# Kernel optimization log

Hardware: AMD Instinct MI355X
Metric: run time of the kernel (lower is better)

## Reference

```python
import jax, jax.numpy as jnp
import numpy as np

B, S, D, H, F = 4, 2048, 1024, 16, 4096
HD = D // H
EPS = 1e-5


def _xavier(key, shape, fan_in, fan_out):
    a = float(np.sqrt(6.0 / (fan_in + fan_out)))
    return jax.random.uniform(key, shape, jnp.float32, -a, a)


def setup_inputs() -> dict:
    key = jax.random.key(0)
    ks = jax.random.split(key, 8)
    x = jax.random.normal(ks[0], (B, S, D), jnp.float32)
    # torch xavier_uniform on (1,H,D,HD) uses fan_in=D, fan_out=HD
    Wq = _xavier(ks[1], (H, D, HD), D, HD)
    Wk = _xavier(ks[2], (H, D, HD), D, HD)
    Wv = _xavier(ks[3], (H, D, HD), D, HD)
    Wo = _xavier(ks[4], (D, D), D, D)
    w_in = _xavier(ks[5], (D, F), D, F)
    b_in = jnp.zeros((F,), jnp.float32)
    w_out = _xavier(ks[6], (F, D), F, D)
    b_out = jnp.zeros((D,), jnp.float32)
    g1 = jnp.ones((D,), jnp.float32)
    be1 = jnp.zeros((D,), jnp.float32)
    g2 = jnp.ones((D,), jnp.float32)
    be2 = jnp.zeros((D,), jnp.float32)
    return {"x": x, "Wq": Wq, "Wk": Wk, "Wv": Wv, "Wo": Wo,
            "g1": g1, "be1": be1, "w_in": w_in, "b_in": b_in,
            "w_out": w_out, "b_out": b_out, "g2": g2, "be2": be2}


def _layernorm(x, g, b):
    mu = jnp.mean(x, axis=-1, keepdims=True)
    var = jnp.mean(jnp.square(x - mu), axis=-1, keepdims=True)
    return (x - mu) * jax.lax.rsqrt(var + EPS) * g + b


def reference(x, Wq, Wk, Wv, Wo, g1, be1, w_in, b_in, w_out, b_out, g2, be2):
    b, s, d = x.shape
    h, _, hd = Wq.shape
    q = jnp.einsum('bsd,hde->bhse', x, Wq)
    k = jnp.einsum('bsd,hde->bhse', x, Wk)
    v = jnp.einsum('bsd,hde->bhse', x, Wv)
    scores = jnp.einsum('bhse,bhte->bhst', q, k) / jnp.sqrt(jnp.float32(hd))
    causal = jnp.triu(jnp.ones((s, s), bool), k=1)  # [S,S]
    scores = jnp.where(causal, -jnp.inf, scores)
    p = jax.nn.softmax(scores, axis=-1)
    attn = jnp.einsum('bhst,bhte->bhse', p, v)
    # torch .view on contiguous (B,H,S,hd) -> (B,S,H*hd): plain reshape (no transpose)
    attn = attn.reshape(b, s, h * hd)
    attn = attn @ Wo
    x = _layernorm(x + attn, g1, be1)
    ffn = jax.nn.relu(x @ w_in + b_in) @ w_out + b_out
    x = _layernorm(x + ffn, g2, be2)
    return x
```

## Files before the change

### kernel.cpp

```cpp
#include <hip/hip_runtime.h>
#include <hip/hip_bf16.h>

typedef __hip_bfloat16 bf16;

#define BB 4
#define SS 2048
#define DD 1024
#define HH 16
#define FF 4096
#define HD 64
#define LN_EPS 1e-5f
#define QSCALE 0.1803368801111204f

typedef __attribute__((ext_vector_type(8))) __bf16 bf16x8;
typedef __attribute__((ext_vector_type(8))) unsigned short u16x8;
typedef __attribute__((ext_vector_type(4))) float f32x4;

__device__ __forceinline__ float cvt(float v) { return v; }
__device__ __forceinline__ float cvt(bf16 v) { return __bfloat162float(v); }
__device__ __forceinline__ void stf(float* p, float v) { *p = v; }
__device__ __forceinline__ void stf(bf16* p, float v) { *p = __float2bfloat16(v); }

__device__ __forceinline__ unsigned short f2bf_rne(float x) {
    unsigned int u = __float_as_uint(x);
    unsigned int r = (u + 0x7fffu + ((u >> 16) & 1u)) >> 16;
    return (unsigned short)r;
}

__device__ __forceinline__ void async_cp16(const void* g, void* l) {
    __builtin_amdgcn_global_load_lds(
        (const __attribute__((address_space(1))) unsigned int*)g,
        (__attribute__((address_space(3))) unsigned int*)l, 16, 0, 0);
}

__device__ __forceinline__ u16x8 ld_f32_chunk(const float* p) {
    const float4* q = (const float4*)p;
    const float4 a = q[0], b = q[1];
    u16x8 r;
    r[0] = f2bf_rne(a.x); r[1] = f2bf_rne(a.y); r[2] = f2bf_rne(a.z); r[3] = f2bf_rne(a.w);
    r[4] = f2bf_rne(b.x); r[5] = f2bf_rne(b.y); r[6] = f2bf_rne(b.z); r[7] = f2bf_rne(b.w);
    return r;
}

template <typename TA, typename TC, int EPI, int BW>
__launch_bounds__(256)
__global__ void mfma_gemm(const TA* __restrict__ A, const bf16* __restrict__ Bt,
                          TC* __restrict__ C, const float* __restrict__ bias,
                          const bf16* __restrict__ resb,
                          bf16* __restrict__ C2, bf16* __restrict__ C3,
                          int M, int N, int K, float oscale) {
    constexpr bool AF = (sizeof(TA) == 4);
    __shared__ unsigned short As[128 * 64];
    __shared__ unsigned short Bs[128 * 64];

    const int tid = threadIdx.x;
    const int lane = tid & 63;
    const int w = tid >> 6;
    const int wm = w >> 1, wn = w & 1;

    const int gx = gridDim.x, gy = gridDim.y;
    const int id = blockIdx.y * gx + blockIdx.x;
    const int R = gy >> 3;
    const int k = id & 7;
    const int j = id >> 3;
    const int sbs = R * BW;
    const int sb = j / sbs;
    const int rem = j % sbs;
    const int by = k * R + rem / BW;
    const int bx = sb * BW + rem % BW;
    const int m0 = by * 128, n0 = bx * 128;

    int ff[4], fr[4], fc[4], fg[4];
#pragma unroll
    for (int i = 0; i < 4; ++i) {
        ff[i] = tid + i * 256;
        fr[i] = ff[i] >> 3;
        fc[i] = ff[i] & 7;
        fg[i] = fc[i] ^ (fr[i] & 7);
    }

    f32x4 acc[4][4];
#pragma unroll
    for (int i = 0; i < 4; ++i)
#pragma unroll
        for (int j2 = 0; j2 < 4; ++j2) acc[i][j2] = (f32x4){0.f, 0.f, 0.f, 0.f};

    u16x8 sa[4];
    if (AF) {
#pragma unroll
        for (int i = 0; i < 4; ++i)
            sa[i] = ld_f32_chunk((const float*)A + (size_t)(m0 + fr[i]) * K + fg[i] * 8);
    }

    for (int k0 = 0; k0 < K; k0 += 64) {
        if (k0 > 0) __syncthreads();
        if (AF) {
#pragma unroll
            for (int i = 0; i < 4; ++i)
                *(u16x8*)&As[ff[i] * 8] = sa[i];
        } else {
#pragma unroll
            for (int i = 0; i < 4; ++i)
                async_cp16((const unsigned short*)A + (size_t)(m0 + fr[i]) * K + k0 + fg[i] * 8,
                           &As[ff[i] * 8]);
        }
#pragma unroll
        for (int i = 0; i < 4; ++i)
            async_cp16((const unsigned short*)Bt + (size_t)(n0 + fr[i]) * K + k0 + fg[i] * 8,
                       &Bs[ff[i] * 8]);
        __syncthreads();

        if (AF && k0 + 64 < K) {
            const int kn = k0 + 64;
#pragma unroll
            for (int i = 0; i < 4; ++i)
                sa[i] = ld_f32_chunk((const float*)A + (size_t)(m0 + fr[i]) * K + kn + fg[i] * 8);
        }

#pragma unroll
        for (int ks = 0; ks < 2; ++ks) {
            bf16x8 af[4], bfr[4];
#pragma unroll
            for (int i = 0; i < 4; ++i) {
                const int row = wm * 64 + i * 16 + (lane & 15);
                const int col = wn * 64 + i * 16 + (lane & 15);
                const int g = ks * 4 + (lane >> 4);
                af[i]  = *(const bf16x8*)&As[row * 64 + (g ^ (row & 7)) * 8];
                bfr[i] = *(const bf16x8*)&Bs[col * 64 + (g ^ (col & 7)) * 8];
            }
#pragma unroll
            for (int i = 0; i < 4; ++i)
#pragma unroll
                for (int j2 = 0; j2 < 4; ++j2)
                    acc[i][j2] = __builtin_amdgcn_mfma_f32_16x16x32_bf16(
                        af[i], bfr[j2], acc[i][j2], 0, 0, 0);
        }
    }

#pragma unroll
    for (int i = 0; i < 4; ++i) {
        const int mrow0 = m0 + wm * 64 + i * 16 + (lane >> 4) * 4;
#pragma unroll
        for (int j2 = 0; j2 < 4; ++j2) {
            const int n = n0 + wn * 64 + j2 * 16 + (lane & 15);
            if (EPI == 5) {
                const int reg = n >> 10;
                const int nn = n & 1023;
                if (reg == 0) {
#pragma unroll
                    for (int r = 0; r < 4; ++r)
                        stf((bf16*)C + (size_t)(mrow0 + r) * 1024 + nn, acc[i][j2][r] * oscale);
                } else if (reg == 1) {
#pragma unroll
                    for (int r = 0; r < 4; ++r)
                        stf(C2 + (size_t)(mrow0 + r) * 1024 + nn, acc[i][j2][r]);
                } else {
                    const int bb = mrow0 >> 11, s = mrow0 & 2047;
                    ushort4 pk;
                    pk.x = f2bf_rne(acc[i][j2][0]);
                    pk.y = f2bf_rne(acc[i][j2][1]);
                    pk.z = f2bf_rne(acc[i][j2][2]);
                    pk.w = f2bf_rne(acc[i][j2][3]);
                    *(ushort4*)((unsigned short*)C3 + ((size_t)bb * 1024 + nn) * SS + s) = pk;
                }
            } else {
#pragma unroll
                for (int r = 0; r < 4; ++r) {
                    const size_t idx = (size_t)(mrow0 + r) * N + n;
                    float v = acc[i][j2][r];
                    if (EPI == 0) v *= oscale;
                    if (EPI == 2) { v += bias[n]; v = fmaxf(v, 0.0f); }
                    if (EPI == 6) v += bias[n] + cvt(resb[idx]);
                    if (EPI == 7) v += cvt(resb[idx]);
                    stf(&C[idx], v);
                }
            }
        }
    }
}

__launch_bounds__(256)
__global__ void prep_kernel(const float* __restrict__ x,
                            const float* __restrict__ Wq, const float* __restrict__ Wk,
                            const float* __restrict__ Wv, const float* __restrict__ Wo,
                            const float* __restrict__ w_in, const float* __restrict__ w_out,
                            bf16* __restrict__ xb, bf16* __restrict__ WqkvT,
                            bf16* __restrict__ WoT, bf16* __restrict__ w_inT,
                            bf16* __restrict__ w_outT) {
    const int id = blockIdx.x;
    if (id < 8192) {
        const int i = id * 256 + threadIdx.x;
        const float4 v = ((const float4*)x)[i];
        ushort4 p;
        p.x = f2bf_rne(v.x); p.y = f2bf_rne(v.y); p.z = f2bf_rne(v.z); p.w = f2bf_rne(v.w);
        ((ushort4*)xb)[i] = p;
        return;
    }
    __shared__ float t[32][33];
    const int rem = id - 8192;
    const float* in;
    bf16* out;
    int R, C, bx, by;
    size_t in_o = 0, out_o = 0;
    if (rem < 3072) {
        const int z = rem >> 6, r2 = rem & 63;
        const int wi = z >> 4, head = z & 15;
        in = (wi == 0) ? Wq : (wi == 1) ? Wk : Wv;
        in_o = (size_t)head * DD * HD;
        out = WqkvT;
        out_o = (size_t)wi * DD * DD + (size_t)head * HD * DD;
        R = DD; C = HD;
        bx = (r2 & 1) * 32; by = (r2 >> 1) * 32;
    } else if (rem < 3072 + 1024) {
        const int r2 = rem - 3072;
        in = Wo; out = WoT; R = DD; C = DD;
        bx = (r2 & 31) * 32; by = (r2 >> 5) * 32;
    } else if (rem < 3072 + 1024 + 4096) {
        const int r2 = rem - 3072 - 1024;
        in = w_in; out = w_inT; R = DD; C = FF;
        bx = (r2 & 127) * 32; by = (r2 >> 7) * 32;
    } else {
        const int r2 = rem - 3072 - 1024 - 4096;
        in = w_out; out = w_outT; R = FF; C = DD;
        bx = (r2 & 31) * 32; by = (r2 >> 5) * 32;
    }
    const int tx = threadIdx.x & 31, ty = threadIdx.x >> 5;
#pragma unroll
    for (int i = 0; i < 32; i += 8)
        t[ty + i][tx] = in[in_o + (size_t)(by + ty + i) * C + bx + tx];
    __syncthreads();
#pragma unroll
    for (int i = 0; i < 32; i += 8)
        out[out_o + (size_t)(bx + ty + i) * R + by + tx] = __float2bfloat16(t[tx][ty + i]);
}

__launch_bounds__(256, 4)
__global__ void attn_mfma(const bf16* __restrict__ Q, const bf16* __restrict__ K,
                          const bf16* __restrict__ VT, bf16* __restrict__ O) {
    __shared__ unsigned short Ks[64 * 64];
    __shared__ unsigned short Vs[64 * 64];
    __shared__ unsigned short Ps[64 * 72];

    const int tid = threadIdx.x;
    const int lane = tid & 63;
    const int w = tid >> 6;
    const int ln = lane & 15;
    const int qd = lane >> 4;
    const int bh = blockIdx.x;
    const int b = bh >> 4;
    const int h = bh & 15;
    const int qi = 31 - blockIdx.y;
    const int q0 = qi * 64;

    bf16x8 aq[2];
    {
        const unsigned short* qp =
            (const unsigned short*)Q + ((size_t)b * SS + q0 + w * 16 + ln) * DD + h * HD;
        aq[0] = *(const bf16x8*)(qp + qd * 8);
        aq[1] = *(const bf16x8*)(qp + 32 + qd * 8);
    }

    int sf[2], sr[2], sg[2];
#pragma unroll
    for (int i = 0; i < 2; ++i) {
        sf[i] = tid + i * 256;
        sr[i] = sf[i] >> 3;
        sg[i] = (sf[i] & 7) ^ (sr[i] & 7);
    }
    const unsigned short* kbase = (const unsigned short*)K + (size_t)b * SS * DD + h * HD;
    const unsigned short* vbase = (const unsigned short*)VT + (size_t)(b * DD + h * HD) * SS;

    f32x4 oacc[4];
#pragma unroll
    for (int e = 0; e < 4; ++e) oacc[e] = (f32x4){0.f, 0.f, 0.f, 0.f};
    float l_r[4] = {0.f, 0.f, 0.f, 0.f};

    for (int kt = 0; kt <= qi; ++kt) {
        const int t0 = kt * 64;
        __syncthreads();
#pragma unroll
        for (int i = 0; i < 2; ++i) {
            async_cp16(kbase + (size_t)(t0 + sr[i]) * DD + sg[i] * 8, &Ks[sf[i] * 8]);
            async_cp16(vbase + (size_t)sr[i] * SS + t0 + sg[i] * 8, &Vs[sf[i] * 8]);
        }
        __syncthreads();

        f32x4 sfr[4];
#pragma unroll
        for (int ct = 0; ct < 4; ++ct) {
            const int row = ct * 16 + ln;
            const bf16x8 b0 = *(const bf16x8*)&Ks[row * 64 + ((qd) ^ (row & 7)) * 8];
            const bf16x8 b1 = *(const bf16x8*)&Ks[row * 64 + ((4 + qd) ^ (row & 7)) * 8];
            f32x4 t = __builtin_amdgcn_mfma_f32_16x16x32_bf16(
                aq[0], b0, (f32x4){0.f, 0.f, 0.f, 0.f}, 0, 0, 0);
            sfr[ct] = __builtin_amdgcn_mfma_f32_16x16x32_bf16(aq[1], b1, t, 0, 0, 0);
        }

        if (kt == qi) {
#pragma unroll
            for (int ct = 0; ct < 4; ++ct) {
                const int tg = t0 + ct * 16 + ln;
#pragma unroll
                for (int r = 0; r < 4; ++r) {
                    const int qg = q0 + w * 16 + qd * 4 + r;
                    if (tg > qg) sfr[ct][r] = -1e30f;
                }
            }
        }

#pragma unroll
        for (int ct = 0; ct < 4; ++ct)
#pragma unroll
            for (int r = 0; r < 4; ++r)
                sfr[ct][r] = __builtin_amdgcn_exp2f(sfr[ct][r]);
#pragma unroll
        for (int r = 0; r < 4; ++r)
            l_r[r] += (sfr[0][r] + sfr[1][r]) + (sfr[2][r] + sfr[3][r]);

#pragma unroll
        for (int ct = 0; ct < 4; ++ct)
#pragma unroll
            for (int r = 0; r < 4; ++r)
                Ps[(w * 16 + qd * 4 + r) * 72 + ct * 16 + ln] = f2bf_rne(sfr[ct][r]);
        const bf16x8 ap0 = *(const bf16x8*)&Ps[(w * 16 + ln) * 72 + qd * 8];
        const bf16x8 ap1 = *(const bf16x8*)&Ps[(w * 16 + ln) * 72 + 32 + qd * 8];

#pragma unroll
        for (int et = 0; et < 4; ++et) {
            const int row = et * 16 + ln;
            const bf16x8 v0 = *(const bf16x8*)&Vs[row * 64 + ((qd) ^ (row & 7)) * 8];
            const bf16x8 v1 = *(const bf16x8*)&Vs[row * 64 + ((4 + qd) ^ (row & 7)) * 8];
            oacc[et] = __builtin_amdgcn_mfma_f32_16x16x32_bf16(ap0, v0, oacc[et], 0, 0, 0);
            oacc[et] = __builtin_amdgcn_mfma_f32_16x16x32_bf16(ap1, v1, oacc[et], 0, 0, 0);
        }
    }

#pragma unroll
    for (int st = 1; st <= 8; st <<= 1)
#pragma unroll
        for (int r = 0; r < 4; ++r)
            l_r[r] += __shfl_xor(l_r[r], st);
    float linv[4];
#pragma unroll
    for (int r = 0; r < 4; ++r) linv[r] = 1.0f / l_r[r];
    unsigned short* ob = (unsigned short*)O + (size_t)bh * SS * HD;
#pragma unroll
    for (int et = 0; et < 4; ++et)
#pragma unroll
        for (int r = 0; r < 4; ++r) {
            const int qg = q0 + w * 16 + qd * 4 + r;
            ob[(size_t)qg * HD + et * 16 + ln] = f2bf_rne(oacc[et][r] * linv[r]);
        }
}

template <typename TIN, typename TOUT>
__launch_bounds__(256)
__global__ void ln_kernel(const TIN* __restrict__ X, TOUT* __restrict__ Y,
                          const float* __restrict__ g, const float* __restrict__ be) {
    const int row = blockIdx.x;
    const int tid = threadIdx.x;
    const int lane = tid & 63, w = tid >> 6;
    __shared__ float red[8];
    __shared__ float mv[2];

    float4 v;
    if (sizeof(TIN) == 4) {
        v = ((const float4*)((const float*)X + (size_t)row * DD))[tid];
    } else {
        const ushort4 u = ((const ushort4*)((const unsigned short*)X + (size_t)row * DD))[tid];
        v.x = __uint_as_float((unsigned)u.x << 16);
        v.y = __uint_as_float((unsigned)u.y << 16);
        v.z = __uint_as_float((unsigned)u.z << 16);
        v.w = __uint_as_float((unsigned)u.w << 16);
    }
    float s = (v.x + v.y) + (v.z + v.w);
    float q = (v.x * v.x + v.y * v.y) + (v.z * v.z + v.w * v.w);
#pragma unroll
    for (int st = 1; st < 64; st <<= 1) {
        s += __shfl_xor(s, st);
        q += __shfl_xor(q, st);
    }
    if (lane == 0) { red[w] = s; red[4 + w] = q; }
    __syncthreads();
    if (tid == 0) {
        const float ts = (red[0] + red[1]) + (red[2] + red[3]);
        const float tq = (red[4] + red[5]) + (red[6] + red[7]);
        const float mu = ts * (1.0f / DD);
        mv[0] = mu;
        mv[1] = rsqrtf(tq * (1.0f / DD) - mu * mu + LN_EPS);
    }
    __syncthreads();
    const float mu = mv[0], rs = mv[1];
    const float4 gg = ((const float4*)g)[tid];
    const float4 bb = ((const float4*)be)[tid];
    float o[4];
    o[0] = (v.x - mu) * rs * gg.x + bb.x;
    o[1] = (v.y - mu) * rs * gg.y + bb.y;
    o[2] = (v.z - mu) * rs * gg.z + bb.z;
    o[3] = (v.w - mu) * rs * gg.w + bb.w;
    if (sizeof(TOUT) == 4) {
        float4 of = {o[0], o[1], o[2], o[3]};
        ((float4*)((float*)Y + (size_t)row * DD))[tid] = of;
    } else {
        ushort4 p;
        p.x = f2bf_rne(o[0]); p.y = f2bf_rne(o[1]);
        p.z = f2bf_rne(o[2]); p.w = f2bf_rne(o[3]);
        ((ushort4*)((unsigned short*)Y + (size_t)row * DD))[tid] = p;
    }
}

extern "C" void kernel_launch(void* const* d_in, const int* in_sizes, int n_in,
                              void* d_out, int out_size, void* d_ws, size_t ws_size,
                              hipStream_t stream) {
    const float* x = (const float*)d_in[0];
    const float* Wq = (const float*)d_in[1];
    const float* Wk = (const float*)d_in[2];
    const float* Wv = (const float*)d_in[3];
    const float* Wo = (const float*)d_in[4];
    const float* g1 = (const float*)d_in[5];
    const float* be1 = (const float*)d_in[6];
    const float* w_in = (const float*)d_in[7];
    const float* b_in = (const float*)d_in[8];
    const float* w_out = (const float*)d_in[9];
    const float* b_out = (const float*)d_in[10];
    const float* g2 = (const float*)d_in[11];
    const float* be2 = (const float*)d_in[12];
    float* out = (float*)d_out;

    char* wsb = (char*)d_ws;
    const size_t MiB = 1u << 20;
    bf16* Qb = (bf16*)(wsb);
    bf16* Kb = (bf16*)(wsb + 16 * MiB);
    bf16* VT = (bf16*)(wsb + 32 * MiB);
    bf16* At = (bf16*)(wsb + 48 * MiB);
    bf16* xb = (bf16*)(wsb + 64 * MiB);
    bf16* X1b = (bf16*)(wsb + 80 * MiB);
    bf16* Hd = (bf16*)(wsb);
    bf16* X2b = (bf16*)(wsb + 64 * MiB);
    bf16* WqkvT = (bf16*)(wsb + 96 * MiB);
    bf16* WoT = (bf16*)(wsb + 102 * MiB);
    bf16* w_inT = (bf16*)(wsb + 104 * MiB);
    bf16* w_outT = (bf16*)(wsb + 112 * MiB);
    (void)ws_size;

    const int M = BB * SS;
    dim3 blk(256);

    prep_kernel<<<dim3(8192 + 3072 + 1024 + 4096 + 4096), blk, 0, stream>>>(
        x, Wq, Wk, Wv, Wo, w_in, w_out, xb, WqkvT, WoT, w_inT, w_outT);

    mfma_gemm<bf16, bf16, 5, 4><<<dim3(3 * DD / 128, M / 128), blk, 0, stream>>>(
        xb, WqkvT, Qb, nullptr, nullptr, Kb, VT, M, 3 * DD, DD, QSCALE);

    attn_mfma<<<dim3(BB * HH, SS / 64), blk, 0, stream>>>(Qb, Kb, VT, At);

    mfma_gemm<bf16, bf16, 7, 8><<<dim3(DD / 128, M / 128), blk, 0, stream>>>(
        At, WoT, X1b, nullptr, xb, nullptr, nullptr, M, DD, DD, 1.0f);
    ln_kernel<bf16, bf16><<<dim3(M), blk, 0, stream>>>(X1b, X1b, g1, be1);

    mfma_gemm<bf16, bf16, 2, 4><<<dim3(FF / 128, M / 128), blk, 0, stream>>>(
        X1b, w_inT, Hd, b_in, nullptr, nullptr, nullptr, M, FF, DD, 1.0f);

    mfma_gemm<bf16, bf16, 6, 8><<<dim3(DD / 128, M / 128), blk, 0, stream>>>(
        Hd, w_outT, X2b, b_out, X1b, nullptr, nullptr, M, DD, FF, 1.0f);

    ln_kernel<bf16, float><<<dim3(M), blk, 0, stream>>>(X2b, out, g2, be2);
}
```

Baseline: 463.9 us.

## Double-buffer K tiles and overlap V loads in attention with vmcnt waits

The attention kernel now double-buffers K in shared memory and prefetches the next K tile while computing on the current one. V for the current tile loads in parallel with the QK^T MFMAs, and fine-grained s_waitcnt vmcnt waits with raw barriers replace the two full __syncthreads per iteration. The aim is to hide global-to-LDS latency behind compute, at the cost of extra LDS and fragile hand-counted wait values. The FFN up-projection GEMM's BW template parameter also changes from 4 to 32.

```diff
diff --git a/kernel.cpp b/kernel.cpp
--- a/kernel.cpp
+++ b/kernel.cpp
@@ -31,6 +31,19 @@
     __builtin_amdgcn_global_load_lds(
         (const __attribute__((address_space(1))) unsigned int*)g,
         (__attribute__((address_space(3))) unsigned int*)l, 16, 0, 0);
+}
+
+template <int N>
+__device__ __forceinline__ void s_wait_vmcnt() {
+    asm volatile("s_waitcnt vmcnt(%0)" ::"n"(N) : "memory");
+    __builtin_amdgcn_sched_barrier(0);
+}
+
+__device__ __forceinline__ void sync_raw() {
+    asm volatile("" ::: "memory");
+    __builtin_amdgcn_s_barrier();
+    asm volatile("" ::: "memory");
+    __builtin_amdgcn_sched_barrier(0);
 }
 
 __device__ __forceinline__ u16x8 ld_f32_chunk(const float* p) {
@@ -237,7 +250,7 @@
 __launch_bounds__(256, 4)
 __global__ void attn_mfma(const bf16* __restrict__ Q, const bf16* __restrict__ K,
                           const bf16* __restrict__ VT, bf16* __restrict__ O) {
-    __shared__ unsigned short Ks[64 * 64];
+    __shared__ unsigned short Ks[2][64 * 64];
     __shared__ unsigned short Vs[64 * 64];
     __shared__ unsigned short Ps[64 * 72];
 
@@ -270,27 +283,44 @@
     const unsigned short* kbase = (const unsigned short*)K + (size_t)b * SS * DD + h * HD;
     const unsigned short* vbase = (const unsigned short*)VT + (size_t)(b * DD + h * HD) * SS;
 
+    auto stageK = [&](int kt, int buf) {
+        const int t0 = kt * 64;
+#pragma unroll
+        for (int i = 0; i < 2; ++i)
+            async_cp16(kbase + (size_t)(t0 + sr[i]) * DD + sg[i] * 8, &Ks[buf][sf[i] * 8]);
+    };
+    auto stageV = [&](int kt) {
+        const int t0 = kt * 64;
+#pragma unroll
+        for (int i = 0; i < 2; ++i)
+            async_cp16(vbase + (size_t)sr[i] * SS + t0 + sg[i] * 8, &Vs[sf[i] * 8]);
+    };
+
     f32x4 oacc[4];
 #pragma unroll
     for (int e = 0; e < 4; ++e) oacc[e] = (f32x4){0.f, 0.f, 0.f, 0.f};
     float l_r[4] = {0.f, 0.f, 0.f, 0.f};
 
+    stageK(0, 0);
+    stageV(0);
+
     for (int kt = 0; kt <= qi; ++kt) {
-        const int t0 = kt * 64;
-        __syncthreads();
-#pragma unroll
-        for (int i = 0; i < 2; ++i) {
-            async_cp16(kbase + (size_t)(t0 + sr[i]) * DD + sg[i] * 8, &Ks[sf[i] * 8]);
-            async_cp16(vbase + (size_t)sr[i] * SS + t0 + sg[i] * 8, &Vs[sf[i] * 8]);
-        }
-        __syncthreads();
+        const int cur = kt & 1;
+        if (kt > 0) stageV(kt);
+        if (kt < qi) {
+            stageK(kt + 1, cur ^ 1);
+            s_wait_vmcnt<4>();
+        } else {
+            s_wait_vmcnt<2>();
+        }
+        sync_raw();
 
         f32x4 sfr[4];
 #pragma unroll
         for (int ct = 0; ct < 4; ++ct) {
             const int row = ct * 16 + ln;
-            const bf16x8 b0 = *(const bf16x8*)&Ks[row * 64 + ((qd) ^ (row & 7)) * 8];
-            const bf16x8 b1 = *(const bf16x8*)&Ks[row * 64 + ((4 + qd) ^ (row & 7)) * 8];
+            const bf16x8 b0 = *(const bf16x8*)&Ks[cur][row * 64 + ((qd) ^ (row & 7)) * 8];
+            const bf16x8 b1 = *(const bf16x8*)&Ks[cur][row * 64 + ((4 + qd) ^ (row & 7)) * 8];
             f32x4 t = __builtin_amdgcn_mfma_f32_16x16x32_bf16(
                 aq[0], b0, (f32x4){0.f, 0.f, 0.f, 0.f}, 0, 0, 0);
             sfr[ct] = __builtin_amdgcn_mfma_f32_16x16x32_bf16(aq[1], b1, t, 0, 0, 0);
@@ -299,7 +329,7 @@
         if (kt == qi) {
 #pragma unroll
             for (int ct = 0; ct < 4; ++ct) {
-                const int tg = t0 + ct * 16 + ln;
+                const int tg = kt * 64 + ct * 16 + ln;
 #pragma unroll
                 for (int r = 0; r < 4; ++r) {
                     const int qg = q0 + w * 16 + qd * 4 + r;
@@ -324,6 +354,10 @@
                 Ps[(w * 16 + qd * 4 + r) * 72 + ct * 16 + ln] = f2bf_rne(sfr[ct][r]);
         const bf16x8 ap0 = *(const bf16x8*)&Ps[(w * 16 + ln) * 72 + qd * 8];
         const bf16x8 ap1 = *(const bf16x8*)&Ps[(w * 16 + ln) * 72 + 32 + qd * 8];
+
+        if (kt < qi) s_wait_vmcnt<2>();
+        else         s_wait_vmcnt<0>();
+        sync_raw();
 
 #pragma unroll
         for (int et = 0; et < 4; ++et) {
@@ -333,6 +367,9 @@
             oacc[et] = __builtin_amdgcn_mfma_f32_16x16x32_bf16(ap0, v0, oacc[et], 0, 0, 0);
             oacc[et] = __builtin_amdgcn_mfma_f32_16x16x32_bf16(ap1, v1, oacc[et], 0, 0, 0);
         }
+
+        asm volatile("s_waitcnt lgkmcnt(0)" ::: "memory");
+        sync_raw();
     }
 
 #pragma unroll
@@ -458,7 +495,7 @@
         At, WoT, X1b, nullptr, xb, nullptr, nullptr, M, DD, DD, 1.0f);
     ln_kernel<bf16, bf16><<<dim3(M), blk, 0, stream>>>(X1b, X1b, g1, be1);
 
-    mfma_gemm<bf16, bf16, 2, 4><<<dim3(FF / 128, M / 128), blk, 0, stream>>>(
+    mfma_gemm<bf16, bf16, 2, 32><<<dim3(FF / 128, M / 128), blk, 0, stream>>>(
         X1b, w_inT, Hd, b_in, nullptr, nullptr, nullptr, M, FF, DD, 1.0f);
 
     mfma_gemm<bf16, bf16, 6, 8><<<dim3(DD / 128, M / 128), blk, 0, stream>>>(
```

After: 446.3 us. 1.04x faster.
